# Kernel tuning notes

Hardware: AMD Instinct MI355X
Metric: run time of the kernel (lower is better)

## Reference

```python
import jax, jax.numpy as jnp
import numpy as np

BATCH = 16384
NNZ = 524288
INPUT_DIM = 30000
OUTPUT_DIM = 300


def setup_inputs() -> dict:
    key = jax.random.key(0)
    k1, k2, k3, k4 = jax.random.split(key, 4)
    sp_rows = jnp.sort(jax.random.randint(k1, (NNZ,), 0, BATCH, dtype=jnp.int32))
    sp_cols = jax.random.randint(k2, (NNZ,), 0, INPUT_DIM, dtype=jnp.int32)
    sp_vals = jax.random.uniform(k3, (NNZ,), dtype=jnp.float32)
    # glorot init for weights, zeros bias (as in the TF module)
    scale = jnp.sqrt(6.0 / (INPUT_DIM + OUTPUT_DIM)).astype(jnp.float32)
    weights = jax.random.uniform(k4, (INPUT_DIM, OUTPUT_DIM), dtype=jnp.float32,
                                 minval=-scale, maxval=scale)
    bias = jnp.zeros((OUTPUT_DIM,), dtype=jnp.float32)
    return {"sp_rows": sp_rows, "sp_cols": sp_cols, "sp_vals": sp_vals,
            "weights": weights, "bias": bias, "batch_size": BATCH}


def reference(sp_rows, sp_cols, sp_vals, weights, bias, batch_size):
    # sparse [batch, input_dim] @ dense [input_dim, output_dim]:
    # gather weight rows per nnz, scale by value, segment-sum into output rows.
    contrib = sp_vals[:, None] * weights[sp_cols]          # [nnz, output_dim]
    dense_vector = jax.ops.segment_sum(contrib, sp_rows,
                                       num_segments=batch_size)  # [batch, output_dim]
    dense_vector = dense_vector + bias
    return jax.nn.relu(dense_vector)
```

## Files before the change

kernel.cpp:

```cpp
#include <hip/hip_runtime.h>

#define OUT_DIM 300

typedef _Float16 half4_t __attribute__((ext_vector_type(4)));
typedef _Float16 half2_t __attribute__((ext_vector_type(2)));

__global__ __launch_bounds__(256) void row_ptr_scatter(
    const int* __restrict__ rows, int* __restrict__ row_ptr, int nnz, int batch)
{
    int i = blockIdx.x * 256 + threadIdx.x;
    if (i >= nnz) return;
    int r = rows[i];
    int prev = (i == 0) ? -1 : rows[i - 1];
    for (int q = prev + 1; q <= r; ++q) row_ptr[q] = i;
    if (i == nnz - 1)
        for (int q = r + 1; q <= batch; ++q) row_ptr[q] = nnz;
}

__global__ __launch_bounds__(256) void repack_f16_sliced(
    const float* __restrict__ w, unsigned char* __restrict__ wf,
    int in_dim, int tierA)
{
    const int PPR = OUT_DIM / 2;
    int i = blockIdx.x * 256 + threadIdx.x;
    if (i >= in_dim * PPR) return;
    int row = i / PPR;
    int p   = i - row * PPR;
    int s   = p / 38;
    int pc  = p - s * 38;
    int stride = tierA ? 160 : ((s == 3) ? 144 : 152);
    size_t sbase = (size_t)s * in_dim * (tierA ? 160 : 152);
    size_t dst = sbase + (size_t)row * stride + (size_t)pc * 4;
    float2 f = *(const float2*)(w + (size_t)row * OUT_DIM + 2 * p);
    half2_t h;
    h.x = (_Float16)f.x;
    h.y = (_Float16)f.y;
    *(half2_t*)(wf + dst) = h;
}

__global__ __launch_bounds__(256) void spmm_sliced3(
    const int* __restrict__ row_ptr,
    const int* __restrict__ cols,
    const float* __restrict__ vals,
    const unsigned char* __restrict__ wf,
    const float* __restrict__ bias,
    float* __restrict__ out,
    int batch, int in_dim, int tierA)
{
    __shared__ uint2 sh[4][76];

    const int slice = blockIdx.x & 3;
    const int wave  = threadIdx.x >> 6;
    const int lane  = threadIdx.x & 63;
    const int row   = (blockIdx.x >> 2) * 4 + wave;
    if (row >= batch) return;

    const int nch    = (slice == 3) ? 18 : 19;
    const int stride = tierA ? 160 : ((slice == 3) ? 144 : 152);
    const unsigned char* wslice = wf + (size_t)slice * in_dim * (tierA ? 160 : 152);

    int grp = lane / nch;
    int ch  = lane - grp * nch;
    const int choff = ch * 8;

    uint2* shw = sh[wave];

    const int lo = row_ptr[row];
    const int hi = row_ptr[row + 1];

    float4 acc = make_float4(0.f, 0.f, 0.f, 0.f);

    for (int base = lo; base < hi; base += 64) {
        const int rem = hi - base;
        const int cnt = rem < 64 ? rem : 64;

        uint2 ov = make_uint2(0u, 0u);
        if (lane < cnt) {
            int c = cols[base + lane];
            ov.x = (unsigned)(c * stride);
            ov.y = __float_as_uint(vals[base + lane]);
        }
        shw[lane] = ov;
        if (lane < 12) shw[64 + lane] = make_uint2(0u, 0u);

        const int rr  = (cnt + 2) / 3;
        const int rrp = (rr + 3) & ~3;
        for (int r0 = 0; r0 < rrp; r0 += 4) {
#pragma unroll
            for (int u = 0; u < 4; ++u) {
                uint2 q = shw[3 * (r0 + u) + grp];
                float v = __uint_as_float(q.y);
                half4_t wv = *(const half4_t*)(wslice + q.x + choff);
                acc.x += v * (float)wv.x;
                acc.y += v * (float)wv.y;
                acc.z += v * (float)wv.z;
                acc.w += v * (float)wv.w;
            }
        }
    }

    float ax = acc.x + __shfl_down(acc.x, nch) + __shfl_down(acc.x, 2 * nch);
    float ay = acc.y + __shfl_down(acc.y, nch) + __shfl_down(acc.y, 2 * nch);
    float az = acc.z + __shfl_down(acc.z, nch) + __shfl_down(acc.z, 2 * nch);
    float aw = acc.w + __shfl_down(acc.w, nch) + __shfl_down(acc.w, 2 * nch);

    if (lane < nch) {
        const int colb = 76 * slice + 4 * lane;
        const float4 b = *(const float4*)(bias + colb);
        float4 rv;
        rv.x = fmaxf(ax + b.x, 0.f);
        rv.y = fmaxf(ay + b.y, 0.f);
        rv.z = fmaxf(az + b.z, 0.f);
        rv.w = fmaxf(aw + b.w, 0.f);
        *(float4*)(out + (size_t)row * OUT_DIM + colb) = rv;
    }
}

__global__ __launch_bounds__(256) void spmm_wave_f32_kernel(
    const int* __restrict__ row_ptr,
    const int* __restrict__ cols,
    const float* __restrict__ vals,
    const float* __restrict__ weights,
    const float* __restrict__ bias,
    float* __restrict__ out,
    int batch)
{
    const int wave = threadIdx.x >> 6;
    const int lane = threadIdx.x & 63;
    const int row  = blockIdx.x * 4 + wave;
    if (row >= batch) return;

    const int lo = row_ptr[row];
    const int hi = row_ptr[row + 1];

    float4 acc0 = make_float4(0.f, 0.f, 0.f, 0.f);
    float4 acc1 = make_float4(0.f, 0.f, 0.f, 0.f);
    const bool tail = (lane < 75 - 64);

    for (int base = lo; base < hi; base += 64) {
        const int rem = hi - base;
        const int cnt = rem < 64 ? rem : 64;
        int   c = 0;
        float v = 0.0f;
        if (lane < cnt) { c = cols[base + lane]; v = vals[base + lane]; }
        const int rounds = (cnt + 7) & ~7;
        for (int k = 0; k < rounds; k += 8) {
#pragma unroll
            for (int u = 0; u < 8; ++u) {
                const int   cc = __shfl(c, k + u);
                const float vv = __shfl(v, k + u);
                const float4* wrow = (const float4*)(weights + (size_t)cc * OUT_DIM);
                float4 w0 = wrow[lane];
                acc0.x += vv * w0.x; acc0.y += vv * w0.y;
                acc0.z += vv * w0.z; acc0.w += vv * w0.w;
                if (tail) {
                    float4 w1 = wrow[64 + lane];
                    acc1.x += vv * w1.x; acc1.y += vv * w1.y;
                    acc1.z += vv * w1.z; acc1.w += vv * w1.w;
                }
            }
        }
    }

    const float4* b4 = (const float4*)bias;
    float4* orow = (float4*)(out + (size_t)row * OUT_DIM);
    float4 b0 = b4[lane];
    float4 r0;
    r0.x = fmaxf(acc0.x + b0.x, 0.f);
    r0.y = fmaxf(acc0.y + b0.y, 0.f);
    r0.z = fmaxf(acc0.z + b0.z, 0.f);
    r0.w = fmaxf(acc0.w + b0.w, 0.f);
    orow[lane] = r0;
    if (tail) {
        float4 b1 = b4[64 + lane];
        float4 r1;
        r1.x = fmaxf(acc1.x + b1.x, 0.f);
        r1.y = fmaxf(acc1.y + b1.y, 0.f);
        r1.z = fmaxf(acc1.z + b1.z, 0.f);
        r1.w = fmaxf(acc1.w + b1.w, 0.f);
        orow[64 + lane] = r1;
    }
}

extern "C" void kernel_launch(void* const* d_in, const int* in_sizes, int n_in,
                              void* d_out, int out_size, void* d_ws, size_t ws_size,
                              hipStream_t stream) {
    const int*   sp_rows = (const int*)d_in[0];
    const int*   sp_cols = (const int*)d_in[1];
    const float* sp_vals = (const float*)d_in[2];
    const float* weights = (const float*)d_in[3];
    const float* bias    = (const float*)d_in[4];
    float* out = (float*)d_out;

    const int nnz    = in_sizes[0];
    const int w_elts = in_sizes[3];
    const int in_dim = w_elts / OUT_DIM;
    const int batch  = out_size / OUT_DIM;

    size_t rp_bytes = (size_t)(batch + 1) * sizeof(int);
    size_t wf_off   = (rp_bytes + 255) & ~(size_t)255;
    size_t needA    = wf_off + (size_t)in_dim * 640 + 256;
    size_t needB    = wf_off + (size_t)in_dim * 600 + 256;

    int* row_ptr = (int*)d_ws;

    row_ptr_scatter<<<(nnz + 255) / 256, 256, 0, stream>>>(
        sp_rows, row_ptr, nnz, batch);

    if (ws_size >= needB) {
        const int tierA = (ws_size >= needA) ? 1 : 0;
        unsigned char* wf = (unsigned char*)d_ws + wf_off;
        const int pairs = in_dim * (OUT_DIM / 2);
        repack_f16_sliced<<<(pairs + 255) / 256, 256, 0, stream>>>(
            weights, wf, in_dim, tierA);
        const int rowgroups = (batch + 3) / 4;
        spmm_sliced3<<<rowgroups * 4, 256, 0, stream>>>(
            row_ptr, sp_cols, sp_vals, wf, bias, out, batch, in_dim, tierA);
    } else {
        spmm_wave_f32_kernel<<<(batch + 3) / 4, 256, 0, stream>>>(
            row_ptr, sp_cols, sp_vals, weights, bias, out, batch);
    }
}
```

Measured before the change: 140.0 us.

## Split fp16 weights into eight 128-byte column slices and fuse setup kernels

Repacks the fp16 weight copy into eight column slices, each with a 128-byte row stride, so every gathered row segment fits one aligned cache line, and computes each output row with eight blocks of half2 loads instead of four blocks of half4 loads. The row-pointer scatter and weight repack are merged into one launch to cut a kernel launch. The cost is twice as many gather instructions per nonzero and a larger padded workspace (1024 bytes per input row). When the workspace is too small, the old four-slice path now always uses the 160-byte stride.

New measurement: 167.8 us. +19.9%, slower.

```diff
diff --git a/kernel.cpp b/kernel.cpp
--- a/kernel.cpp
+++ b/kernel.cpp
@@ -2,8 +2,124 @@
 
 #define OUT_DIM 300
 
+typedef _Float16 half2_t __attribute__((ext_vector_type(2)));
 typedef _Float16 half4_t __attribute__((ext_vector_type(4)));
-typedef _Float16 half2_t __attribute__((ext_vector_type(2)));
+
+__global__ __launch_bounds__(256) void setup8_kernel(
+    const int* __restrict__ rows, int* __restrict__ row_ptr,
+    const float* __restrict__ w, unsigned char* __restrict__ wf,
+    int nnz, int batch, int in_dim, int scat_blocks)
+{
+    if ((int)blockIdx.x < scat_blocks) {
+        int i = blockIdx.x * 256 + threadIdx.x;
+        if (i >= nnz) return;
+        int r = rows[i];
+        int prev = (i == 0) ? -1 : rows[i - 1];
+        for (int q = prev + 1; q <= r; ++q) row_ptr[q] = i;
+        if (i == nnz - 1)
+            for (int q = r + 1; q <= batch; ++q) row_ptr[q] = nnz;
+        return;
+    }
+    const int UPR = OUT_DIM / 2;
+    int j = ((int)blockIdx.x - scat_blocks) * 256 + threadIdx.x;
+    if (j >= in_dim * UPR) return;
+    int r = j / UPR;
+    int k = j - r * UPR;
+    int s = k / 19;
+    int kc = k - s * 19;
+    float2 f = *(const float2*)(w + (size_t)r * OUT_DIM + 2 * k);
+    half2_t h;
+    h.x = (_Float16)f.x;
+    h.y = (_Float16)f.y;
+    *(half2_t*)(wf + ((size_t)s * in_dim + r) * 128 + kc * 4) = h;
+}
+
+__global__ __launch_bounds__(256) void spmm8(
+    const int* __restrict__ row_ptr,
+    const int* __restrict__ cols,
+    const float* __restrict__ vals,
+    const unsigned char* __restrict__ wf,
+    const float* __restrict__ bias,
+    float* __restrict__ out,
+    int batch, int in_dim)
+{
+    __shared__ uint2 sh[4][76];
+
+    const int slice = blockIdx.x & 7;
+    const int wave  = threadIdx.x >> 6;
+    const int lane  = threadIdx.x & 63;
+    const int row   = (blockIdx.x >> 3) * 4 + wave;
+    if (row >= batch) return;
+
+    const int grp = lane / 19;
+    const int ch  = lane - grp * 19;
+    const int choff = ch * 4;
+
+    const unsigned char* wslice = wf + (size_t)slice * in_dim * 128;
+    uint2* shw = sh[wave];
+
+    const int lo = row_ptr[row];
+    const int hi = row_ptr[row + 1];
+
+    float2 acc = make_float2(0.f, 0.f);
+
+    for (int base = lo; base < hi; base += 64) {
+        const int rem = hi - base;
+        const int cnt = rem < 64 ? rem : 64;
+
+        uint2 ov = make_uint2(0u, 0u);
+        if (lane < cnt) {
+            ov.x = (unsigned)cols[base + lane] << 7;
+            ov.y = __float_as_uint(vals[base + lane]);
+        }
+        shw[lane] = ov;
+        if (lane < 12) shw[64 + lane] = make_uint2(0u, 0u);
+
+        const int rr  = (cnt + 2) / 3;
+        const int rrp = (rr + 7) & ~7;
+        for (int r0 = 0; r0 < rrp; r0 += 8) {
+#pragma unroll
+            for (int u = 0; u < 8; ++u) {
+                uint2 q = shw[3 * (r0 + u) + grp];
+                float v = __uint_as_float(q.y);
+                half2_t wv = *(const half2_t*)(wslice + q.x + choff);
+                acc.x += v * (float)wv.x;
+                acc.y += v * (float)wv.y;
+            }
+        }
+    }
+
+    float ax = acc.x + __shfl_down(acc.x, 19) + __shfl_down(acc.x, 38);
+    float ay = acc.y + __shfl_down(acc.y, 19) + __shfl_down(acc.y, 38);
+
+    const int nch = (slice == 7) ? 17 : 19;
+    if (lane < nch) {
+        const int col = slice * 38 + 2 * lane;
+        const float2 b = *(const float2*)(bias + col);
+        float2 rv;
+        rv.x = fmaxf(ax + b.x, 0.f);
+        rv.y = fmaxf(ay + b.y, 0.f);
+        *(float2*)(out + (size_t)row * OUT_DIM + col) = rv;
+    }
+}
+
+__global__ __launch_bounds__(256) void repack_f16_sliced(
+    const float* __restrict__ w, unsigned char* __restrict__ wf, int in_dim)
+{
+    const int PPR = OUT_DIM / 2;
+    int i = blockIdx.x * 256 + threadIdx.x;
+    if (i >= in_dim * PPR) return;
+    int row = i / PPR;
+    int p   = i - row * PPR;
+    int s   = p / 38;
+    int pc  = p - s * 38;
+    size_t dst = (size_t)s * in_dim * 160 + (size_t)row * 160 + (size_t)pc * 4;
+    float2 f = *(const float2*)(w + (size_t)row * OUT_DIM + 2 * p);
+    half2_t h;
+    h.x = (_Float16)f.x;
+    h.y = (_Float16)f.y;
+    *(half2_t*)(wf + dst) = h;
+}
 
 __global__ __launch_bounds__(256) void row_ptr_scatter(
     const int* __restrict__ rows, int* __restrict__ row_ptr, int nnz, int batch)
@@ -17,27 +133,6 @@
         for (int q = r + 1; q <= batch; ++q) row_ptr[q] = nnz;
 }
 
-__global__ __launch_bounds__(256) void repack_f16_sliced(
-    const float* __restrict__ w, unsigned char* __restrict__ wf,
-    int in_dim, int tierA)
-{
-    const int PPR = OUT_DIM / 2;
-    int i = blockIdx.x * 256 + threadIdx.x;
-    if (i >= in_dim * PPR) return;
-    int row = i / PPR;
-    int p   = i - row * PPR;
-    int s   = p / 38;
-    int pc  = p - s * 38;
-    int stride = tierA ? 160 : ((s == 3) ? 144 : 152);
-    size_t sbase = (size_t)s * in_dim * (tierA ? 160 : 152);
-    size_t dst = sbase + (size_t)row * stride + (size_t)pc * 4;
-    float2 f = *(const float2*)(w + (size_t)row * OUT_DIM + 2 * p);
-    half2_t h;
-    h.x = (_Float16)f.x;
-    h.y = (_Float16)f.y;
-    *(half2_t*)(wf + dst) = h;
-}
-
 __global__ __launch_bounds__(256) void spmm_sliced3(
     const int* __restrict__ row_ptr,
     const int* __restrict__ cols,
@@ -45,7 +140,7 @@
     const unsigned char* __restrict__ wf,
     const float* __restrict__ bias,
     float* __restrict__ out,
-    int batch, int in_dim, int tierA)
+    int batch, int in_dim)
 {
     __shared__ uint2 sh[4][76];
 
@@ -55,29 +150,24 @@
     const int row   = (blockIdx.x >> 2) * 4 + wave;
     if (row >= batch) return;
 
-    const int nch    = (slice == 3) ? 18 : 19;
-    const int stride = tierA ? 160 : ((slice == 3) ? 144 : 152);
-    const unsigned char* wslice = wf + (size_t)slice * in_dim * (tierA ? 160 : 152);
+    const int nch = (slice == 3) ? 18 : 19;
+    const unsigned char* wslice = wf + (size_t)slice * in_dim * 160;
 
     int grp = lane / nch;
     int ch  = lane - grp * nch;
     const int choff = ch * 8;
-
     uint2* shw = sh[wave];
 
     const int lo = row_ptr[row];
     const int hi = row_ptr[row + 1];
-
     float4 acc = make_float4(0.f, 0.f, 0.f, 0.f);
 
     for (int base = lo; base < hi; base += 64) {
         const int rem = hi - base;
         const int cnt = rem < 64 ? rem : 64;
-
         uint2 ov = make_uint2(0u, 0u);
         if (lane < cnt) {
-            int c = cols[base + lane];
-            ov.x = (unsigned)(c * stride);
+            ov.x = (unsigned)(cols[base + lane] * 160);
             ov.y = __float_as_uint(vals[base + lane]);
         }
         shw[lane] = ov;
@@ -132,7 +222,6 @@
 
     const int lo = row_ptr[row];
     const int hi = row_ptr[row + 1];
-
     float4 acc0 = make_float4(0.f, 0.f, 0.f, 0.f);
     float4 acc1 = make_float4(0.f, 0.f, 0.f, 0.f);
     const bool tail = (lane < 75 - 64);
@@ -199,24 +288,32 @@
 
     size_t rp_bytes = (size_t)(batch + 1) * sizeof(int);
     size_t wf_off   = (rp_bytes + 255) & ~(size_t)255;
-    size_t needA    = wf_off + (size_t)in_dim * 640 + 256;
-    size_t needB    = wf_off + (size_t)in_dim * 600 + 256;
+    size_t need8    = wf_off + (size_t)in_dim * 8 * 128 + 256;
+    size_t need4    = wf_off + (size_t)in_dim * 4 * 160 + 256;
 
     int* row_ptr = (int*)d_ws;
-
-    row_ptr_scatter<<<(nnz + 255) / 256, 256, 0, stream>>>(
-        sp_rows, row_ptr, nnz, batch);
-
-    if (ws_size >= needB) {
-        const int tierA = (ws_size >= needA) ? 1 : 0;
+    const int rowgroups = (batch + 3) / 4;
+
+    if (ws_size >= need8) {
         unsigned char* wf = (unsigned char*)d_ws + wf_off;
+        const int scat_blocks = (nnz + 255) / 256;
+        const int rep_blocks  = (in_dim * (OUT_DIM / 2) + 255) / 256;
+        setup8_kernel<<<scat_blocks + rep_blocks, 256, 0, stream>>>(
+            sp_rows, row_ptr, weights, wf, nnz, batch, in_dim, scat_blocks);
+        spmm8<<<rowgroups * 8, 256, 0, stream>>>(
+            row_ptr, sp_cols, sp_vals, wf, bias, out, batch, in_dim);
+    } else if (ws_size >= need4) {
+        unsigned char* wf = (unsigned char*)d_ws + wf_off;
+        row_ptr_scatter<<<(nnz + 255) / 256, 256, 0, stream>>>(
+            sp_rows, row_ptr, nnz, batch);
         const int pairs = in_dim * (OUT_DIM / 2);
         repack_f16_sliced<<<(pairs + 255) / 256, 256, 0, stream>>>(
-            weights, wf, in_dim, tierA);
-        const int rowgroups = (batch + 3) / 4;
+            weights, wf, in_dim);
         spmm_sliced3<<<rowgroups * 4, 256, 0, stream>>>(
-            row_ptr, sp_cols, sp_vals, wf, bias, out, batch, in_dim, tierA);
+            row_ptr, sp_cols, sp_vals, wf, bias, out, batch, in_dim);
     } else {
+        row_ptr_scatter<<<(nnz + 255) / 256, 256, 0, stream>>>(
+            sp_rows, row_ptr, nnz, batch);
         spmm_wave_f32_kernel<<<(batch + 3) / 4, 256, 0, stream>>>(
             row_ptr, sp_cols, sp_vals, weights, bias, out, batch);
     }
```

## Fuse setup kernels and widen SpMM gathers to 16-byte fp16 loads

Applied to the files above, without the earlier changes.

Merges the row-pointer scatter and the fp16 weight repack into one launch, which removes a kernel launch and its dependency gap. The repacked weights now use a uniform 160-byte stride with 80-column slices. The SpMM kernel has each lane gather 8 halves (16 bytes) instead of 4, and runs 6 nnz groups of 10 lanes with a two-stage shuffle reduction. The aim is fewer, wider memory transactions per nonzero, at the cost of more accumulator registers, an extra reduction step, and 4 idle lanes per wave.

New measurement: 137.5 us. Within noise of the previous version (-1.7%).

```diff
diff --git a/kernel.cpp b/kernel.cpp
--- a/kernel.cpp
+++ b/kernel.cpp
@@ -2,8 +2,137 @@
 
 #define OUT_DIM 300
 
-typedef _Float16 half4_t __attribute__((ext_vector_type(4)));
 typedef _Float16 half2_t __attribute__((ext_vector_type(2)));
+typedef _Float16 half8_t __attribute__((ext_vector_type(8)));
+
+__global__ __launch_bounds__(256) void setup4_kernel(
+    const int* __restrict__ rows, int* __restrict__ row_ptr,
+    const float* __restrict__ w, unsigned char* __restrict__ wf,
+    int nnz, int batch, int in_dim, int scat_blocks)
+{
+    if ((int)blockIdx.x < scat_blocks) {
+        int i = blockIdx.x * 256 + threadIdx.x;
+        if (i >= nnz) return;
+        int r = rows[i];
+        int prev = (i == 0) ? -1 : rows[i - 1];
+        for (int q = prev + 1; q <= r; ++q) row_ptr[q] = i;
+        if (i == nnz - 1)
+            for (int q = r + 1; q <= batch; ++q) row_ptr[q] = nnz;
+        return;
+    }
+    const int UPR = OUT_DIM / 2;
+    int j = ((int)blockIdx.x - scat_blocks) * 256 + threadIdx.x;
+    if (j >= in_dim * UPR) return;
+    int r = j / UPR;
+    int k = j - r * UPR;
+    int s = k / 40; if (s > 3) s = 3;
+    int kc = k - 40 * s;
+    float2 f = *(const float2*)(w + (size_t)r * OUT_DIM + 2 * k);
+    half2_t h;
+    h.x = (_Float16)f.x;
+    h.y = (_Float16)f.y;
+    *(half2_t*)(wf + ((size_t)s * in_dim + r) * 160 + kc * 4) = h;
+}
+
+__global__ __launch_bounds__(256) void spmm4w(
+    const int* __restrict__ row_ptr,
+    const int* __restrict__ cols,
+    const float* __restrict__ vals,
+    const unsigned char* __restrict__ wf,
+    const float* __restrict__ bias,
+    float* __restrict__ out,
+    int batch, int in_dim)
+{
+    __shared__ uint2 sh[4][76];
+
+    const int slice = blockIdx.x & 3;
+    const int wave  = threadIdx.x >> 6;
+    const int lane  = threadIdx.x & 63;
+    const int row   = (blockIdx.x >> 2) * 4 + wave;
+    if (row >= batch) return;
+
+    const int grp = lane / 10;
+    const int ch  = lane - grp * 10;
+    const int choff = ch * 16;
+
+    const unsigned char* wslice = wf + (size_t)slice * in_dim * 160;
+    uint2* shw = sh[wave];
+
+    if (lane < 12) shw[64 + lane] = make_uint2(0u, 0u);
+
+    const int lo = row_ptr[row];
+    const int hi = row_ptr[row + 1];
+
+    float a0 = 0.f, a1 = 0.f, a2 = 0.f, a3 = 0.f;
+    float a4 = 0.f, a5 = 0.f, a6 = 0.f, a7 = 0.f;
+
+    for (int base = lo; base < hi; base += 64) {
+        const int rem = hi - base;
+        const int cnt = rem < 64 ? rem : 64;
+
+        uint2 ov = make_uint2(0u, 0u);
+        if (lane < cnt) {
+            ov.x = (unsigned)(cols[base + lane] * 160);
+            ov.y = __float_as_uint(vals[base + lane]);
+        }
+        shw[lane] = ov;
+
+        const int rr  = (cnt + 5) / 6;
+        const int rrp = (rr + 3) & ~3;
+        for (int r0 = 0; r0 < rrp; r0 += 4) {
+#pragma unroll
+            for (int u = 0; u < 4; ++u) {
+                uint2 q = shw[6 * (r0 + u) + grp];
+                float v = __uint_as_float(q.y);
+                half8_t wv = *(const half8_t*)(wslice + q.x + choff);
+                a0 += v * (float)wv[0];
+                a1 += v * (float)wv[1];
+                a2 += v * (float)wv[2];
+                a3 += v * (float)wv[3];
+                a4 += v * (float)wv[4];
+                a5 += v * (float)wv[5];
+                a6 += v * (float)wv[6];
+                a7 += v * (float)wv[7];
+            }
+        }
+    }
+
+    a0 += __shfl_down(a0, 30); a1 += __shfl_down(a1, 30);
+    a2 += __shfl_down(a2, 30); a3 += __shfl_down(a3, 30);
+    a4 += __shfl_down(a4, 30); a5 += __shfl_down(a5, 30);
+    a6 += __shfl_down(a6, 30); a7 += __shfl_down(a7, 30);
+
+    float f0 = a0 + __shfl_down(a0, 10) + __shfl_down(a0, 20);
+    float f1 = a1 + __shfl_down(a1, 10) + __shfl_down(a1, 20);
+    float f2 = a2 + __shfl_down(a2, 10) + __shfl_down(a2, 20);
+    float f3 = a3 + __shfl_down(a3, 10) + __shfl_down(a3, 20);
+    float f4 = a4 + __shfl_down(a4, 10) + __shfl_down(a4, 20);
+    float f5 = a5 + __shfl_down(a5, 10) + __shfl_down(a5, 20);
+    float f6 = a6 + __shfl_down(a6, 10) + __shfl_down(a6, 20);
+    float f7 = a7 + __shfl_down(a7, 10) + __shfl_down(a7, 20);
+
+    const int nlan = (slice == 3) ? 8 : 10;
+    if (lane < nlan) {
+        const int col = slice * 80 + lane * 8;
+        float* orow = out + (size_t)row * OUT_DIM + col;
+        const float4 b0 = *(const float4*)(bias + col);
+        float4 s0;
+        s0.x = fmaxf(f0 + b0.x, 0.f);
+        s0.y = fmaxf(f1 + b0.y, 0.f);
+        s0.z = fmaxf(f2 + b0.z, 0.f);
+        s0.w = fmaxf(f3 + b0.w, 0.f);
+        *(float4*)orow = s0;
+        if (slice < 3 || lane < 7) {
+            const float4 b1 = *(const float4*)(bias + col + 4);
+            float4 s1;
+            s1.x = fmaxf(f4 + b1.x, 0.f);
+            s1.y = fmaxf(f5 + b1.y, 0.f);
+            s1.z = fmaxf(f6 + b1.z, 0.f);
+            s1.w = fmaxf(f7 + b1.w, 0.f);
+            *(float4*)(orow + 4) = s1;
+        }
+    }
+}
 
 __global__ __launch_bounds__(256) void row_ptr_scatter(
     const int* __restrict__ rows, int* __restrict__ row_ptr, int nnz, int batch)
@@ -15,105 +144,6 @@
     for (int q = prev + 1; q <= r; ++q) row_ptr[q] = i;
     if (i == nnz - 1)
         for (int q = r + 1; q <= batch; ++q) row_ptr[q] = nnz;
-}
-
-__global__ __launch_bounds__(256) void repack_f16_sliced(
-    const float* __restrict__ w, unsigned char* __restrict__ wf,
-    int in_dim, int tierA)
-{
-    const int PPR = OUT_DIM / 2;
-    int i = blockIdx.x * 256 + threadIdx.x;
-    if (i >= in_dim * PPR) return;
-    int row = i / PPR;
-    int p   = i - row * PPR;
-    int s   = p / 38;
-    int pc  = p - s * 38;
-    int stride = tierA ? 160 : ((s == 3) ? 144 : 152);
-    size_t sbase = (size_t)s * in_dim * (tierA ? 160 : 152);
-    size_t dst = sbase + (size_t)row * stride + (size_t)pc * 4;
-    float2 f = *(const float2*)(w + (size_t)row * OUT_DIM + 2 * p);
-    half2_t h;
-    h.x = (_Float16)f.x;
-    h.y = (_Float16)f.y;
-    *(half2_t*)(wf + dst) = h;
-}
-
-__global__ __launch_bounds__(256) void spmm_sliced3(
-    const int* __restrict__ row_ptr,
-    const int* __restrict__ cols,
-    const float* __restrict__ vals,
-    const unsigned char* __restrict__ wf,
-    const float* __restrict__ bias,
-    float* __restrict__ out,
-    int batch, int in_dim, int tierA)
-{
-    __shared__ uint2 sh[4][76];
-
-    const int slice = blockIdx.x & 3;
-    const int wave  = threadIdx.x >> 6;
-    const int lane  = threadIdx.x & 63;
-    const int row   = (blockIdx.x >> 2) * 4 + wave;
-    if (row >= batch) return;
-
-    const int nch    = (slice == 3) ? 18 : 19;
-    const int stride = tierA ? 160 : ((slice == 3) ? 144 : 152);
-    const unsigned char* wslice = wf + (size_t)slice * in_dim * (tierA ? 160 : 152);
-
-    int grp = lane / nch;
-    int ch  = lane - grp * nch;
-    const int choff = ch * 8;
-
-    uint2* shw = sh[wave];
-
-    const int lo = row_ptr[row];
-    const int hi = row_ptr[row + 1];
-
-    float4 acc = make_float4(0.f, 0.f, 0.f, 0.f);
-
-    for (int base = lo; base < hi; base += 64) {
-        const int rem = hi - base;
-        const int cnt = rem < 64 ? rem : 64;
-
-        uint2 ov = make_uint2(0u, 0u);
-        if (lane < cnt) {
-            int c = cols[base + lane];
-            ov.x = (unsigned)(c * stride);
-            ov.y = __float_as_uint(vals[base + lane]);
-        }
-        shw[lane] = ov;
-        if (lane < 12) shw[64 + lane] = make_uint2(0u, 0u);
-
-        const int rr  = (cnt + 2) / 3;
-        const int rrp = (rr + 3) & ~3;
-        for (int r0 = 0; r0 < rrp; r0 += 4) {
-#pragma unroll
-            for (int u = 0; u < 4; ++u) {
-                uint2 q = shw[3 * (r0 + u) + grp];
-                float v = __uint_as_float(q.y);
-                half4_t wv = *(const half4_t*)(wslice + q.x + choff);
-                acc.x += v * (float)wv.x;
-                acc.y += v * (float)wv.y;
-                acc.z += v * (float)wv.z;
-                acc.w += v * (float)wv.w;
-            }
-        }
-    }
-
-    float ax = acc.x + __shfl_down(acc.x, nch) + __shfl_down(acc.x, 2 * nch);
-    float ay = acc.y + __shfl_down(acc.y, nch) + __shfl_down(acc.y, 2 * nch);
-    float az = acc.z + __shfl_down(acc.z, nch) + __shfl_down(acc.z, 2 * nch);
-    float aw = acc.w + __shfl_down(acc.w, nch) + __shfl_down(acc.w, 2 * nch);
-
-    if (lane < nch) {
-        const int colb = 76 * slice + 4 * lane;
-        const float4 b = *(const float4*)(bias + colb);
-        float4 rv;
-        rv.x = fmaxf(ax + b.x, 0.f);
-        rv.y = fmaxf(ay + b.y, 0.f);
-        rv.z = fmaxf(az + b.z, 0.f);
-        rv.w = fmaxf(aw + b.w, 0.f);
-        *(float4*)(out + (size_t)row * OUT_DIM + colb) = rv;
-    }
 }
 
 __global__ __launch_bounds__(256) void spmm_wave_f32_kernel(
@@ -132,7 +162,6 @@
 
     const int lo = row_ptr[row];
     const int hi = row_ptr[row + 1];
-
     float4 acc0 = make_float4(0.f, 0.f, 0.f, 0.f);
     float4 acc1 = make_float4(0.f, 0.f, 0.f, 0.f);
     const bool tail = (lane < 75 - 64);
@@ -199,24 +228,22 @@
 
     size_t rp_bytes = (size_t)(batch + 1) * sizeof(int);
     size_t wf_off   = (rp_bytes + 255) & ~(size_t)255;
-    size_t needA    = wf_off + (size_t)in_dim * 640 + 256;
-    size_t needB    = wf_off + (size_t)in_dim * 600 + 256;
+    size_t need4    = wf_off + (size_t)in_dim * 4 * 160 + 256;
 
     int* row_ptr = (int*)d_ws;
-
-    row_ptr_scatter<<<(nnz + 255) / 256, 256, 0, stream>>>(
-        sp_rows, row_ptr, nnz, batch);
-
-    if (ws_size >= needB) {
-        const int tierA = (ws_size >= needA) ? 1 : 0;
+    const int rowgroups = (batch + 3) / 4;
+
+    if (ws_size >= need4) {
         unsigned char* wf = (unsigned char*)d_ws + wf_off;
-        const int pairs = in_dim * (OUT_DIM / 2);
-        repack_f16_sliced<<<(pairs + 255) / 256, 256, 0, stream>>>(
-            weights, wf, in_dim, tierA);
-        const int rowgroups = (batch + 3) / 4;
-        spmm_sliced3<<<rowgroups * 4, 256, 0, stream>>>(
-            row_ptr, sp_cols, sp_vals, wf, bias, out, batch, in_dim, tierA);
+        const int scat_blocks = (nnz + 255) / 256;
+        const int rep_blocks  = (in_dim * (OUT_DIM / 2) + 255) / 256;
+        setup4_kernel<<<scat_blocks + rep_blocks, 256, 0, stream>>>(
+            sp_rows, row_ptr, weights, wf, nnz, batch, in_dim, scat_blocks);
+        spmm4w<<<rowgroups * 4, 256, 0, stream>>>(
+            row_ptr, sp_cols, sp_vals, wf, bias, out, batch, in_dim);
     } else {
+        row_ptr_scatter<<<(nnz + 255) / 256, 256, 0, stream>>>(
+            sp_rows, row_ptr, nnz, batch);
         spmm_wave_f32_kernel<<<(batch + 3) / 4, 256, 0, stream>>>(
             row_ptr, sp_cols, sp_vals, weights, bias, out, batch);
     }
```
